# Kernel tuning notes

Hardware: AMD Instinct MI355X
Metric: run time of the kernel (lower is better)

## Reference

```python
import jax, jax.numpy as jnp
import numpy as np

B, S, D, H, DFF = 4, 2048, 1024, 16, 4096
DK = D // H
EPS = 1e-6


def setup_inputs() -> dict:
    key = jax.random.key(0)
    ks = jax.random.split(key, 20)
    p = lambda k, shape: jax.random.normal(k, shape, dtype=jnp.float32) * 0.02
    inp = {
        "x": jax.random.normal(ks[0], (B, S, D), dtype=jnp.float32),
        "src_mask": jax.random.randint(ks[1], (B, 1, 1, S), 0, 2, dtype=jnp.int32),
        "Wq": p(ks[2], (D, D)), "bq": jnp.zeros((D,), jnp.float32),
        "Wk": p(ks[3], (D, D)), "bk": jnp.zeros((D,), jnp.float32),
        "Wv": p(ks[4], (D, D)), "bv": jnp.zeros((D,), jnp.float32),
        "Wo": p(ks[5], (D, D)), "bo": jnp.zeros((D,), jnp.float32),
        "W1": p(ks[6], (D, DFF)), "b1": jnp.zeros((DFF,), jnp.float32),
        "W2": p(ks[7], (DFF, D)), "b2": jnp.zeros((D,), jnp.float32),
        "ln1_a": jnp.ones((D,), jnp.float32), "ln1_b": jnp.zeros((D,), jnp.float32),
        "ln2_a": jnp.ones((D,), jnp.float32), "ln2_b": jnp.zeros((D,), jnp.float32),
    }
    return inp


def _layer_norm(x, a, b):
    # Faithful to source: unbiased std (torch default) and divide by (std + eps)
    mean = jnp.mean(x, axis=-1, keepdims=True)
    std = jnp.std(x, axis=-1, ddof=1, keepdims=True)
    return a * (x - mean) / (std + EPS) + b


def reference(x, src_mask, Wq, bq, Wk, bk, Wv, bv, Wo, bo, W1, b1, W2, b2,
              ln1_a, ln1_b, ln2_a, ln2_b):
    # Multi-head self-attention (dropout = identity, eval mode)
    q = (x @ Wq + bq).reshape(B, S, H, DK)
    k = (x @ Wk + bk).reshape(B, S, H, DK)
    v = (x @ Wv + bv).reshape(B, S, H, DK)
    scores = jnp.einsum("bqhd,bkhd->bhqk", q, k) / jnp.sqrt(jnp.float32(DK))
    scores = jnp.where(src_mask == 0, jnp.float32(-1e9), scores)
    attn = jax.nn.softmax(scores, axis=-1)
    ctx = jnp.einsum("bhqk,bkhd->bqhd", attn, v).reshape(B, S, D)
    attn_out = ctx @ Wo + bo

    x = _layer_norm(x + attn_out, ln1_a, ln1_b)

    # FeedForward: linear -> relu -> (dropout=identity) -> linear
    ff = jax.nn.relu(x @ W1 + b1) @ W2 + b2
    x = _layer_norm(x + ff, ln2_a, ln2_b)
    return x
```

## Files before the change

kernel.cpp:

```cpp
#include <hip/hip_runtime.h>

#define Bn 4
#define Sn 2048
#define Dn 1024
#define Hn 16
#define DKn 64
#define DFFn 4096
#define Mn (Bn * Sn)
#define QKVS 3072

typedef __bf16 bf16;
typedef __attribute__((ext_vector_type(8))) __bf16 bf16x8;
typedef __attribute__((ext_vector_type(4))) __bf16 bf16x4;
typedef __attribute__((ext_vector_type(8))) unsigned short u16x8;
typedef __attribute__((ext_vector_type(4))) float f32x4;
typedef __attribute__((ext_vector_type(16))) float f32x16;

#define LOG2E_DIV8 0.18033688011112042f

__device__ __forceinline__ float exp2fast(float x) {
  return __builtin_amdgcn_exp2f(x);
}

__device__ __forceinline__ void glds16(const bf16* g, bf16* l) {
  __builtin_amdgcn_global_load_lds((const __attribute__((address_space(1))) void*)g,
                                   (__attribute__((address_space(3))) void*)l, 16, 0, 0);
}

__device__ __forceinline__ unsigned int pkbf16(float a, float b) {
  union { __bf16 h[2]; unsigned int u; } x;
  x.h[0] = (__bf16)a; x.h[1] = (__bf16)b;
  return x.u;
}

__device__ __host__ __forceinline__ int bperm(int nl) {
  int wn = nl >> 6, rem = nl & 63, nf = rem >> 4, l = rem & 15;
  return ((nf >> 1) << 7) + (wn << 5) + ((nf & 1) << 4) + l;
}

__global__ __launch_bounds__(256) void k_cvt_bf16(const float* __restrict__ in,
                                                  bf16* __restrict__ out) {
  size_t i = ((size_t)blockIdx.x * 256 + threadIdx.x) * 8;
  f32x4 a = *(const f32x4*)(in + i);
  f32x4 b = *(const f32x4*)(in + i + 4);
  bf16x8 o;
#pragma unroll
  for (int j = 0; j < 4; ++j) { o[j] = (bf16)a[j]; o[j + 4] = (bf16)b[j]; }
  *(bf16x8*)(out + i) = o;
}

__global__ __launch_bounds__(256) void k_prep(const float* __restrict__ Wq,
                                              const float* __restrict__ Wk,
                                              const float* __restrict__ Wv,
                                              const float* __restrict__ Wo,
                                              const float* __restrict__ W1,
                                              const float* __restrict__ W2,
                                              const float* __restrict__ bq,
                                              const float* __restrict__ bk,
                                              const float* __restrict__ bv,
                                              bf16* __restrict__ wqkvT,
                                              bf16* __restrict__ woT,
                                              bf16* __restrict__ w1T,
                                              bf16* __restrict__ w2T,
                                              float* __restrict__ bqkv) {
  __shared__ float tile[32][33];
  const int id = blockIdx.x, t = threadIdx.x;
  if (id >= 12288) {
    int j = (id - 12288) * 256 + t;
    float v = (j < 1024) ? bq[j] * LOG2E_DIV8
            : (j < 2048) ? bk[j - 1024] : bv[j - 2048];
    bqkv[j] = v;
    return;
  }
  const float* in;
  bf16* out;
  int K, N, bx, by, perm;
  float scale = 1.f;
  if (id < 4096) {
    int z = id >> 10, local = id & 1023;
    bx = local & 31; by = local >> 5;
    K = Dn; N = Dn;
    if (z == 0)      { in = Wq; out = wqkvT; scale = LOG2E_DIV8; perm = 1; }
    else if (z == 1) { in = Wk; out = wqkvT + (size_t)1024 * Dn; perm = 1; }
    else if (z == 2) { in = Wv; out = wqkvT + (size_t)2048 * Dn; perm = 1; }
    else             { in = Wo; out = woT; perm = 0; }
  } else if (id < 8192) {
    int local = id - 4096;
    bx = local & 127; by = local >> 7;
    K = Dn; N = DFFn; in = W1; out = w1T; perm = 1;
  } else {
    int local = id - 8192;
    bx = local & 31; by = local >> 5;
    K = DFFn; N = Dn; in = W2; out = w2T; perm = 0;
  }
  const int n0 = bx * 32, k0 = by * 32;
  const int tx = t & 31, ty = t >> 5;
#pragma unroll
  for (int j = ty; j < 32; j += 8)
    tile[j][tx] = in[(size_t)(k0 + j) * N + n0 + tx];
  __syncthreads();
#pragma unroll
  for (int j = ty; j < 32; j += 8) {
    int row = n0 + j;
    if (perm) row = (row & ~255) | bperm(row & 255);
    out[(size_t)row * K + k0 + tx] = (bf16)(tile[tx][j] * scale);
  }
}

__global__ __launch_bounds__(256) void k_vt(const bf16* __restrict__ v,
                                            bf16* __restrict__ vT, int vs) {
  __shared__ bf16 T[64][72];
  const int t = threadIdx.x;
  const int s0 = blockIdx.x * 64;
  const int bh = blockIdx.y, b = bh >> 4, h = bh & 15;
#pragma unroll
  for (int it = 0; it < 2; ++it) {
    int r = (t >> 3) + it * 32;
    int c = t & 7;
    u16x8 val = *(const u16x8*)(v + (size_t)(b * Sn + s0 + r) * vs + h * 64 + c * 8);
    *(u16x8*)&T[r][c * 8] = val;
  }
  __syncthreads();
#pragma unroll
  for (int it = 0; it < 2; ++it) {
    int d = (t >> 3) + it * 32;
    int cs = t & 7;
    bf16x8 o;
#pragma unroll
    for (int j = 0; j < 8; ++j) o[j] = T[cs * 8 + j][d];
    *(bf16x8*)(vT + ((size_t)bh * 64 + d) * Sn + s0 + cs * 8) = o;
  }
}

template <int DO_RELU>
__global__ __launch_bounds__(512, 2) void k_gemm8ph(const bf16* __restrict__ A,
                                                    const bf16* __restrict__ BT,
                                                    const float* __restrict__ bias,
                                                    bf16* __restrict__ C,
                                                    int Ndim, int Kdim) {
  __shared__ __align__(128) bf16 Asm[2][256 * 64];
  __shared__ __align__(128) bf16 Bsm[2][256 * 64];
  const int tid = threadIdx.x;
  const int wid = tid >> 6, lane = tid & 63;
  const int l15 = lane & 15, l4 = lane >> 4;
  const int wm = wid >> 2, wn = wid & 3;

  const int gx = gridDim.x;
  int lin = blockIdx.y * gx + blockIdx.x;
  const int nwg = gx * gridDim.y;
  lin = (lin & 7) * (nwg >> 3) + (lin >> 3);
  const int m0 = (lin / gx) * 256;
  const int n0 = (lin % gx) * 256;

  f32x4 acc[8][4];
#pragma unroll
  for (int mf = 0; mf < 8; ++mf)
#pragma unroll
    for (int nf = 0; nf < 4; ++nf) acc[mf][nf] = f32x4{0.f, 0.f, 0.f, 0.f};

  const int lr = lane >> 3, lc = lane & 7;
  const int NT = Kdim >> 6;
  const int ch0 = lc ^ lr;

#define STGA(buf, t, it)                                                          \
  glds16(A + (size_t)(m0 + (it) * 64 + wid * 8 + lr) * Kdim + (size_t)(t) * 64 +  \
             ch0 * 8,                                                             \
         &Asm[buf][((it) * 64 + wid * 8) * 64]);
#define STGB(buf, t, it)                                                          \
  glds16(BT + (size_t)(n0 + (it) * 64 + wid * 8 + lr) * Kdim + (size_t)(t) * 64 + \
              ch0 * 8,                                                            \
         &Bsm[buf][((it) * 64 + wid * 8) * 64]);

  STGA(0, 0, 0); STGA(0, 0, 2);
  STGB(0, 0, 0); STGB(0, 0, 1);
  STGA(0, 0, 1); STGA(0, 0, 3);
  STGB(0, 0, 2); STGB(0, 0, 3);

  bf16x8 af[4][2], bl[2][2], bh2[2][2];

  for (int j = 0; j < NT; ++j) {
    const int d = j & 1, nb = d ^ 1;
    const bool st = (j + 1 < NT);

    asm volatile("s_waitcnt vmcnt(4)" ::: "memory");
    __builtin_amdgcn_sched_barrier(0);
    __builtin_amdgcn_s_barrier();
#pragma unroll
    for (int mf = 0; mf < 4; ++mf)
#pragma unroll
      for (int kk = 0; kk < 2; ++kk) {
        int row = wm * 128 + mf * 16 + l15;
        int ch = (kk * 4 + l4) ^ (row & 7);
        af[mf][kk] = *(const bf16x8*)&Asm[d][row * 64 + ch * 8];
      }
#pragma unroll
    for (int nf = 0; nf < 2; ++nf)
#pragma unroll
      for (int kk = 0; kk < 2; ++kk) {
        int row = wn * 32 + nf * 16 + l15;
        int ch = (kk * 4 + l4) ^ (row & 7);
        bl[nf][kk] = *(const bf16x8*)&Bsm[d][row * 64 + ch * 8];
      }
    if (st) { STGA(nb, j + 1, 0); STGA(nb, j + 1, 2); }
    __builtin_amdgcn_s_setprio(1);
#pragma unroll
    for (int mf = 0; mf < 4; ++mf)
#pragma unroll
      for (int nf = 0; nf < 2; ++nf)
#pragma unroll
        for (int kk = 0; kk < 2; ++kk)
          acc[mf][nf] = __builtin_amdgcn_mfma_f32_16x16x32_bf16(af[mf][kk], bl[nf][kk],
                                                                acc[mf][nf], 0, 0, 0);
    __builtin_amdgcn_s_setprio(0);

    if (st) asm volatile("s_waitcnt vmcnt(4)" ::: "memory");
    else    asm volatile("s_waitcnt vmcnt(2)" ::: "memory");
    __builtin_amdgcn_sched_barrier(0);
    __builtin_amdgcn_s_barrier();
#pragma unroll
    for (int mf = 0; mf < 4; ++mf)
#pragma unroll
      for (int kk = 0; kk < 2; ++kk) {
        int row = wm * 128 + 64 + mf * 16 + l15;
        int ch = (kk * 4 + l4) ^ (row & 7);
        af[mf][kk] = *(const bf16x8*)&Asm[d][row * 64 + ch * 8];
      }
    if (st) { STGB(nb, j + 1, 0); STGB(nb, j + 1, 1); }
    __builtin_amdgcn_s_setprio(1);
#pragma unroll
    for (int mf = 0; mf < 4; ++mf)
#pragma unroll
      for (int nf = 0; nf < 2; ++nf)
#pragma unroll
        for (int kk = 0; kk < 2; ++kk)
          acc[4 + mf][nf] = __builtin_amdgcn_mfma_f32_16x16x32_bf16(af[mf][kk], bl[nf][kk],
                                                                    acc[4 + mf][nf], 0, 0, 0);
    __builtin_amdgcn_s_setprio(0);

    if (st) asm volatile("s_waitcnt vmcnt(4)" ::: "memory");
    else    asm volatile("s_waitcnt vmcnt(0)" ::: "memory");
    __builtin_amdgcn_sched_barrier(0);
    __builtin_amdgcn_s_barrier();
#pragma unroll
    for (int nf = 0; nf < 2; ++nf)
#pragma unroll
      for (int kk = 0; kk < 2; ++kk) {
        int row = 128 + wn * 32 + nf * 16 + l15;
        int ch = (kk * 4 + l4) ^ (row & 7);
        bh2[nf][kk] = *(const bf16x8*)&Bsm[d][row * 64 + ch * 8];
      }
    if (st) { STGA(nb, j + 1, 1); STGA(nb, j + 1, 3); }
    __builtin_amdgcn_s_setprio(1);
#pragma unroll
    for (int mf = 0; mf < 4; ++mf)
#pragma unroll
      for (int nf = 0; nf < 2; ++nf)
#pragma unroll
        for (int kk = 0; kk < 2; ++kk)
          acc[4 + mf][2 + nf] = __builtin_amdgcn_mfma_f32_16x16x32_bf16(
              af[mf][kk], bh2[nf][kk], acc[4 + mf][2 + nf], 0, 0, 0);
    __builtin_amdgcn_s_setprio(0);

#pragma unroll
    for (int mf = 0; mf < 4; ++mf)
#pragma unroll
      for (int kk = 0; kk < 2; ++kk) {
        int row = wm * 128 + mf * 16 + l15;
        int ch = (kk * 4 + l4) ^ (row & 7);
        af[mf][kk] = *(const bf16x8*)&Asm[d][row * 64 + ch * 8];
      }
    if (st) { STGB(nb, j + 1, 2); STGB(nb, j + 1, 3); }
    __builtin_amdgcn_s_setprio(1);
#pragma unroll
    for (int mf = 0; mf < 4; ++mf)
#pragma unroll
      for (int nf = 0; nf < 2; ++nf)
#pragma unroll
        for (int kk = 0; kk < 2; ++kk)
          acc[mf][2 + nf] = __builtin_amdgcn_mfma_f32_16x16x32_bf16(
              af[mf][kk], bh2[nf][kk], acc[mf][2 + nf], 0, 0, 0);
    __builtin_amdgcn_s_setprio(0);
  }
#undef STGA
#undef STGB

#pragma unroll
  for (int mf = 0; mf < 8; ++mf)
#pragma unroll
    for (int nf = 0; nf < 4; ++nf) {
      int c = n0 + wn * 64 + nf * 16 + l15;
      float bv = bias[c];
      int r0 = m0 + wm * 128 + mf * 16 + l4 * 4;
#pragma unroll
      for (int r = 0; r < 4; ++r) {
        float val = acc[mf][nf][r] + bv;
        if (DO_RELU) val = fmaxf(val, 0.f);
        C[(size_t)(r0 + r) * Ndim + c] = (bf16)val;
      }
    }
}

template <int NFRAG, int DO_RELU>
__global__ __launch_bounds__(512, 2) void k_gemm256(const bf16* __restrict__ A,
                                                    const bf16* __restrict__ BT,
                                                    const float* __restrict__ bias,
                                                    bf16* __restrict__ C,
                                                    int Ndim, int Kdim) {
  __shared__ __align__(128) bf16 Asm[2][256 * 64];
  __shared__ __align__(128) bf16 Bsm[2][NFRAG * 64 * 64];
  const int tid = threadIdx.x;
  const int wid = tid >> 6, lane = tid & 63;
  const int l15 = lane & 15, l4 = lane >> 4;
  const int wm = wid >> 2, wn = wid & 3;

  const int gx = gridDim.x;
  int lin = blockIdx.y * gx + blockIdx.x;
  const int nwg = gx * gridDim.y;
  lin = (lin & 7) * (nwg >> 3) + (lin >> 3);
  const int m0 = (lin / gx) * 256;
  const int n0 = (lin % gx) * (NFRAG * 64);

  f32x4 acc[8][NFRAG];
#pragma unroll
  for (int mf = 0; mf < 8; ++mf)
#pragma unroll
    for (int nf = 0; nf < NFRAG; ++nf) acc[mf][nf] = f32x4{0.f, 0.f, 0.f, 0.f};

  const int lr = lane >> 3, lc = lane & 7;
  const int NT = Kdim >> 6;

#define STAGE(buf, t)                                                              \
  {                                                                                \
    _Pragma("unroll") for (int it = 0; it < 4; ++it) {                             \
      int r = it * 64 + wid * 8 + lr;                                              \
      int ch = lc ^ (r & 7);                                                       \
      glds16(A + (size_t)(m0 + r) * Kdim + (size_t)(t) * 64 + ch * 8,              \
             &Asm[buf][(it * 64 + wid * 8) * 64]);                                 \
    }                                                                              \
    _Pragma("unroll") for (int it = 0; it < NFRAG; ++it) {                         \
      int r = it * 64 + wid * 8 + lr;                                              \
      int ch = lc ^ (r & 7);                                                       \
      glds16(BT + (size_t)(n0 + r) * Kdim + (size_t)(t) * 64 + ch * 8,             \
             &Bsm[buf][(it * 64 + wid * 8) * 64]);                                 \
    }                                                                              \
  }

  int p = 0;
  STAGE(0, 0);
  for (int t = 0; t < NT; ++t) {
    if (t + 1 < NT) {
      STAGE(p ^ 1, t + 1);
      if constexpr (NFRAG == 4) asm volatile("s_waitcnt vmcnt(8)" ::: "memory");
      else                      asm volatile("s_waitcnt vmcnt(6)" ::: "memory");
    } else {
      asm volatile("s_waitcnt vmcnt(0)" ::: "memory");
    }
    __builtin_amdgcn_sched_barrier(0);
    __builtin_amdgcn_s_barrier();

    bf16x8 bfrag[NFRAG][2];
#pragma unroll
    for (int nf = 0; nf < NFRAG; ++nf)
#pragma unroll
      for (int kk = 0; kk < 2; ++kk) {
        int r = wn * (NFRAG * 16) + nf * 16 + l15;
        int ch = (kk * 4 + l4) ^ (r & 7);
        bfrag[nf][kk] = *(const bf16x8*)&Bsm[p][r * 64 + ch * 8];
      }
#pragma unroll
    for (int half = 0; half < 2; ++half) {
      bf16x8 afr[4][2];
#pragma unroll
      for (int mf4 = 0; mf4 < 4; ++mf4)
#pragma unroll
        for (int kk = 0; kk < 2; ++kk) {
          int r = wm * 128 + half * 64 + mf4 * 16 + l15;
          int ch = (kk * 4 + l4) ^ (r & 7);
          afr[mf4][kk] = *(const bf16x8*)&Asm[p][r * 64 + ch * 8];
        }
      __builtin_amdgcn_s_setprio(1);
#pragma unroll
      for (int mf4 = 0; mf4 < 4; ++mf4)
#pragma unroll
        for (int nf = 0; nf < NFRAG; ++nf)
#pragma unroll
          for (int kk = 0; kk < 2; ++kk)
            acc[half * 4 + mf4][nf] = __builtin_amdgcn_mfma_f32_16x16x32_bf16(
                afr[mf4][kk], bfrag[nf][kk], acc[half * 4 + mf4][nf], 0, 0, 0);
      __builtin_amdgcn_s_setprio(0);
    }
    __builtin_amdgcn_s_barrier();
    p ^= 1;
  }
#undef STAGE

#pragma unroll
  for (int mf = 0; mf < 8; ++mf)
#pragma unroll
    for (int nf = 0; nf < NFRAG; ++nf) {
      int c = n0 + wn * (NFRAG * 16) + nf * 16 + l15;
      float bv = bias[c];
      int r0 = m0 + wm * 128 + mf * 16 + l4 * 4;
#pragma unroll
      for (int r = 0; r < 4; ++r) {
        float val = acc[mf][nf][r] + bv;
        if (DO_RELU) val = fmaxf(val, 0.f);
        C[(size_t)(r0 + r) * Ndim + c] = (bf16)val;
      }
    }
}

__global__ __launch_bounds__(512) void k_attn(const bf16* __restrict__ q,
                                              const bf16* __restrict__ k,
                                              const bf16* __restrict__ vT,
                                              const int* __restrict__ mask,
                                              bf16* __restrict__ ctx, int qs) {
  __shared__ __align__(128) bf16 Kt[2][64 * 64];
  __shared__ __align__(128) bf16 Vt[2][64 * 64];
  __shared__ float Mb[Sn];
  const int tid = threadIdx.x, wid = tid >> 6, lane = tid & 63;
  const int q31 = lane & 31, hi = lane >> 5;

  int lin = blockIdx.y * gridDim.x + blockIdx.x;
  lin = (lin & 7) * 64 + (lin >> 3);
  const int qblk = lin & 7, bh = lin >> 3;
  const int b = bh >> 4, h = bh & 15;
  const int q0 = qblk * 256 + wid * 32;

  for (int i = tid; i < Sn; i += 512)
    Mb[i] = mask[b * Sn + i] ? 0.f : -1.44269504e9f;

  bf16x8 qf[4];
#pragma unroll
  for (int t = 0; t < 4; ++t)
    qf[t] = *(const bf16x8*)(q + (size_t)(b * Sn + q0 + q31) * qs + h * 64 +
                             t * 16 + hi * 8);

  f32x16 o[2];
  o[0] = {}; o[1] = {};
  float mr = -INFINITY, lr = 0.f;

  const int lrow = lane >> 3;
  const int lch0 = lane & 7;
  const int sch = lch0 ^ (lrow ^ (wid & 3));

  for (int kb = 0; kb < Sn / 64; ++kb) {
    const int cur = kb & 1;
    if (kb == 0) {
      int row = wid * 8 + lrow;
      glds16(k + (size_t)(b * Sn + row) * qs + h * 64 + sch * 8, &Kt[0][wid * 512]);
      glds16(vT + ((size_t)bh * 64 + row) * Sn + sch * 8, &Vt[0][wid * 512]);
      __syncthreads();
    }
    if (kb + 1 < Sn / 64) {
      int row = wid * 8 + lrow;
      glds16(k + (size_t)(b * Sn + (kb + 1) * 64 + row) * qs + h * 64 + sch * 8,
             &Kt[cur ^ 1][wid * 512]);
      glds16(vT + ((size_t)bh * 64 + row) * Sn + (kb + 1) * 64 + sch * 8,
             &Vt[cur ^ 1][wid * 512]);
    }

    f32x16 sc[2];
#pragma unroll
    for (int kf = 0; kf < 2; ++kf)
#pragma unroll
      for (int rg = 0; rg < 4; ++rg) {
        f32x4 mb4 = *(const f32x4*)&Mb[kb * 64 + kf * 32 + rg * 8 + 4 * hi];
#pragma unroll
        for (int j = 0; j < 4; ++j) sc[kf][rg * 4 + j] = mb4[j];
      }
#pragma unroll
    for (int t = 0; t < 4; ++t) {
#pragma unroll
      for (int kf = 0; kf < 2; ++kf) {
        int row = kf * 32 + q31;
        int ch = (t * 2 + hi) ^ ((row & 7) ^ ((row >> 3) & 3));
        bf16x8 kfr = *(const bf16x8*)&Kt[cur][row * 64 + ch * 8];
        sc[kf] = __builtin_amdgcn_mfma_f32_32x32x16_bf16(kfr, qf[t], sc[kf], 0, 0, 0);
      }
    }

    float rmax = fmaxf(sc[0][0], sc[0][1]);
#pragma unroll
    for (int i = 2; i < 16; i += 2)
      rmax = fmaxf(fmaxf(rmax, sc[0][i]), sc[0][i + 1]);
#pragma unroll
    for (int i = 0; i < 16; i += 2)
      rmax = fmaxf(fmaxf(rmax, sc[1][i]), sc[1][i + 1]);
    rmax = fmaxf(rmax, __shfl_xor(rmax, 32));

    if (!__all(rmax <= mr + 8.f)) {
      float mnew = fmaxf(mr, rmax);
      float psc = exp2fast(mr - mnew);
      mr = mnew;
      lr *= psc;
#pragma unroll
      for (int af = 0; af < 2; ++af)
#pragma unroll
        for (int i = 0; i < 16; ++i) o[af][i] *= psc;
    }

    float psum = 0.f;
#pragma unroll
    for (int kf = 0; kf < 2; ++kf)
#pragma unroll
      for (int i = 0; i < 16; ++i) {
        float p = exp2fast(sc[kf][i] - mr);
        sc[kf][i] = p;
        psum += p;
      }
    psum += __shfl_xor(psum, 32);
    lr += psum;

#pragma unroll
    for (int ks = 0; ks < 4; ++ks) {
      const int kf = ks >> 1, R = (ks & 1) * 8;
      unsigned int a0 = pkbf16(sc[kf][R + 0], sc[kf][R + 1]);
      unsigned int a1 = pkbf16(sc[kf][R + 2], sc[kf][R + 3]);
      unsigned int b0 = pkbf16(sc[kf][R + 4], sc[kf][R + 5]);
      unsigned int b1 = pkbf16(sc[kf][R + 6], sc[kf][R + 7]);
      unsigned int sxa0 = __shfl_xor(a0, 32), sxa1 = __shfl_xor(a1, 32);
      unsigned int sxb0 = __shfl_xor(b0, 32), sxb1 = __shfl_xor(b1, 32);
      union { unsigned int w[4]; bf16x8 v; } pfu;
      pfu.w[0] = hi ? sxb0 : a0;
      pfu.w[1] = hi ? sxb1 : a1;
      pfu.w[2] = hi ? b0 : sxa0;
      pfu.w[3] = hi ? b1 : sxa1;
#pragma unroll
      for (int af = 0; af < 2; ++af) {
        int row = af * 32 + q31;
        int ch = (ks * 2 + hi) ^ ((row & 7) ^ ((row >> 3) & 3));
        bf16x8 vfr = *(const bf16x8*)&Vt[cur][row * 64 + ch * 8];
        o[af] = __builtin_amdgcn_mfma_f32_32x32x16_bf16(vfr, pfu.v, o[af], 0, 0, 0);
      }
    }
    __syncthreads();
  }

  float inv = 1.f / lr;
  const size_t cbase = (size_t)(b * Sn + q0 + q31) * Dn + h * 64;
#pragma unroll
  for (int af = 0; af < 2; ++af)
#pragma unroll
    for (int rg = 0; rg < 4; ++rg) {
      bf16x4 ov;
#pragma unroll
      for (int j = 0; j < 4; ++j) ov[j] = (bf16)(o[af][rg * 4 + j] * inv);
      *(bf16x4*)(ctx + cbase + af * 32 + rg * 8 + 4 * hi) = ov;
    }
}

template <int XF32, int OUTF32>
__global__ __launch_bounds__(256) void k_ln(const void* __restrict__ xp,
                                            const bf16* __restrict__ res,
                                            const float* __restrict__ gamma,
                                            const float* __restrict__ beta,
                                            void* __restrict__ yout) {
  const int row = blockIdx.x, t = threadIdx.x;
  const size_t base = (size_t)row * Dn + t * 4;
  f32x4 a;
  if constexpr (XF32) {
    a = *(const f32x4*)((const float*)xp + base);
  } else {
    bf16x4 x4 = *(const bf16x4*)((const bf16*)xp + base);
#pragma unroll
    for (int j = 0; j < 4; ++j) a[j] = (float)x4[j];
  }
  bf16x4 rb = *(const bf16x4*)(res + base);
  f32x4 vv;
#pragma unroll
  for (int j = 0; j < 4; ++j) vv[j] = a[j] + (float)rb[j];

  float s = vv[0] + vv[1] + vv[2] + vv[3];
#pragma unroll
  for (int off = 32; off; off >>= 1) s += __shfl_xor(s, off);
  __shared__ float red1[4], red2[4];
  if ((t & 63) == 0) red1[t >> 6] = s;
  __syncthreads();
  float mean = (red1[0] + red1[1] + red1[2] + red1[3]) * (1.f / 1024.f);

  float d[4], s2 = 0.f;
#pragma unroll
  for (int j = 0; j < 4; ++j) { d[j] = vv[j] - mean; s2 += d[j] * d[j]; }
#pragma unroll
  for (int off = 32; off; off >>= 1) s2 += __shfl_xor(s2, off);
  if ((t & 63) == 0) red2[t >> 6] = s2;
  __syncthreads();
  float var = (red2[0] + red2[1] + red2[2] + red2[3]) * (1.f / 1023.f);
  float inv = 1.f / (sqrtf(var) + 1e-6f);

  f32x4 g = *(const f32x4*)(gamma + t * 4);
  f32x4 bt = *(const f32x4*)(beta + t * 4);
#pragma unroll
  for (int j = 0; j < 4; ++j) d[j] = g[j] * d[j] * inv + bt[j];
  if constexpr (OUTF32) {
    f32x4 outv = {d[0], d[1], d[2], d[3]};
    *(f32x4*)((float*)yout + base) = outv;
  } else {
    bf16x4 outb;
#pragma unroll
    for (int j = 0; j < 4; ++j) outb[j] = (bf16)d[j];
    *(bf16x4*)((bf16*)yout + base) = outb;
  }
}

extern "C" void kernel_launch(void* const* d_in, const int* in_sizes, int n_in,
                              void* d_out, int out_size, void* d_ws, size_t ws_size,
                              hipStream_t stream) {
  const float* x   = (const float*)d_in[0];
  const int*   msk = (const int*)d_in[1];
  const float* Wq  = (const float*)d_in[2];
  const float* bq  = (const float*)d_in[3];
  const float* Wk  = (const float*)d_in[4];
  const float* bk  = (const float*)d_in[5];
  const float* Wv  = (const float*)d_in[6];
  const float* bv  = (const float*)d_in[7];
  const float* Wo  = (const float*)d_in[8];
  const float* bo  = (const float*)d_in[9];
  const float* W1  = (const float*)d_in[10];
  const float* b1  = (const float*)d_in[11];
  const float* W2  = (const float*)d_in[12];
  const float* b2  = (const float*)d_in[13];
  const float* g1  = (const float*)d_in[14];
  const float* be1 = (const float*)d_in[15];
  const float* g2  = (const float*)d_in[16];
  const float* be2 = (const float*)d_in[17];
  float* out = (float*)d_out;

  char* w = (char*)d_ws;
  size_t off = 0;
  auto alloc = [&](size_t bytes) { void* p = w + off; off += (bytes + 255) & ~(size_t)255; return p; };
  bf16* xb    = (bf16*)alloc((size_t)Mn * Dn * 2);
  bf16* wqkvT = (bf16*)alloc((size_t)QKVS * Dn * 2);
  bf16* woT   = (bf16*)alloc((size_t)Dn * Dn * 2);
  bf16* w1T   = (bf16*)alloc((size_t)Dn * DFFn * 2);
  bf16* w2T   = (bf16*)alloc((size_t)DFFn * Dn * 2);
  float* bqkv = (float*)alloc((size_t)QKVS * 4);
  bf16* qkv   = (bf16*)alloc((size_t)Mn * QKVS * 2);
  bf16* ctx   = (bf16*)alloc((size_t)Mn * Dn * 2);
  bf16* attnb = (bf16*)alloc((size_t)Mn * Dn * 2);
  bf16* yb    = (bf16*)alloc((size_t)Mn * Dn * 2);
  (void)ws_size; (void)in_sizes; (void)n_in; (void)out_size;
  bf16* vT = xb;
  bf16* hh = qkv;
  bf16* ff = xb;

  k_cvt_bf16<<<(Mn * Dn) / 2048, 256, 0, stream>>>(x, xb);
  k_prep<<<12300, 256, 0, stream>>>(Wq, Wk, Wv, Wo, W1, W2, bq, bk, bv,
                                    wqkvT, woT, w1T, w2T, bqkv);

  k_gemm8ph<0><<<dim3(QKVS / 256, Mn / 256), 512, 0, stream>>>(xb, wqkvT, bqkv, qkv, QKVS, Dn);

  k_vt<<<dim3(Sn / 64, Bn * Hn), 256, 0, stream>>>(qkv + 2048, vT, QKVS);
  k_attn<<<dim3(Sn / 256, Bn * Hn), 512, 0, stream>>>(qkv, qkv + 1024, vT, msk, ctx, QKVS);

  k_gemm256<2, 0><<<dim3(Dn / 128, Mn / 256), 512, 0, stream>>>(ctx, woT, bo, attnb, Dn, Dn);

  k_ln<1, 0><<<Mn, 256, 0, stream>>>(x, attnb, g1, be1, yb);

  k_gemm8ph<1><<<dim3(DFFn / 256, Mn / 256), 512, 0, stream>>>(yb, w1T, b1, hh, DFFn, Dn);

  k_gemm256<2, 0><<<dim3(Dn / 128, Mn / 256), 512, 0, stream>>>(hh, w2T, b2, ff, Dn, DFFn);

  k_ln<0, 1><<<Mn, 256, 0, stream>>>(yb, ff, g2, be2, out);
}
```

Measured before the change: 399.0 us.

## Split attention KV range in two halves and merge with combine kernel

Applies a flash-decoding-style split: each attention block now processes half of the key/value sequence, doubling the grid from 512 to 1024 blocks, and writes unnormalized partial outputs plus running max/sum. A new combine kernel rescales and merges the two partials into the normalized context. This aims to improve occupancy and load balance across the GPU's compute units, at the cost of extra partial-output traffic (bf16 partials, extra rounding) and one more kernel launch.

```diff
diff --git a/kernel.cpp b/kernel.cpp
--- a/kernel.cpp
+++ b/kernel.cpp
@@ -414,7 +414,8 @@
                                               const bf16* __restrict__ k,
                                               const bf16* __restrict__ vT,
                                               const int* __restrict__ mask,
-                                              bf16* __restrict__ ctx, int qs) {
+                                              bf16* __restrict__ opart,
+                                              float2* __restrict__ ml, int qs) {
   __shared__ __align__(128) bf16 Kt[2][64 * 64];
   __shared__ __align__(128) bf16 Vt[2][64 * 64];
   __shared__ float Mb[Sn];
@@ -422,10 +423,12 @@
   const int q31 = lane & 31, hi = lane >> 5;
 
   int lin = blockIdx.y * gridDim.x + blockIdx.x;
-  lin = (lin & 7) * 64 + (lin >> 3);
-  const int qblk = lin & 7, bh = lin >> 3;
+  lin = (lin & 7) * 128 + (lin >> 3);
+  const int xq = lin & 15, bh = lin >> 4;
+  const int half = xq & 1, qblk = xq >> 1;
   const int b = bh >> 4, h = bh & 15;
   const int q0 = qblk * 256 + wid * 32;
+  const int kv0 = half * 16;
 
   for (int i = tid; i < Sn; i += 512)
     Mb[i] = mask[b * Sn + i] ? 0.f : -1.44269504e9f;
@@ -444,15 +447,17 @@
   const int lch0 = lane & 7;
   const int sch = lch0 ^ (lrow ^ (wid & 3));
 
-  for (int kb = 0; kb < Sn / 64; ++kb) {
-    const int cur = kb & 1;
-    if (kb == 0) {
+  for (int t16 = 0; t16 < 16; ++t16) {
+    const int kb = kv0 + t16;
+    const int cur = t16 & 1;
+    if (t16 == 0) {
       int row = wid * 8 + lrow;
-      glds16(k + (size_t)(b * Sn + row) * qs + h * 64 + sch * 8, &Kt[0][wid * 512]);
-      glds16(vT + ((size_t)bh * 64 + row) * Sn + sch * 8, &Vt[0][wid * 512]);
+      glds16(k + (size_t)(b * Sn + kb * 64 + row) * qs + h * 64 + sch * 8,
+             &Kt[0][wid * 512]);
+      glds16(vT + ((size_t)bh * 64 + row) * Sn + kb * 64 + sch * 8, &Vt[0][wid * 512]);
       __syncthreads();
     }
-    if (kb + 1 < Sn / 64) {
+    if (t16 + 1 < 16) {
       int row = wid * 8 + lrow;
       glds16(k + (size_t)(b * Sn + (kb + 1) * 64 + row) * qs + h * 64 + sch * 8,
              &Kt[cur ^ 1][wid * 512]);
@@ -537,17 +542,40 @@
     __syncthreads();
   }
 
-  float inv = 1.f / lr;
-  const size_t cbase = (size_t)(b * Sn + q0 + q31) * Dn + h * 64;
+  const size_t row = (size_t)(b * Sn + q0 + q31);
+  const size_t obase = ((size_t)half * Mn + row) * Dn + h * 64;
 #pragma unroll
   for (int af = 0; af < 2; ++af)
 #pragma unroll
     for (int rg = 0; rg < 4; ++rg) {
       bf16x4 ov;
 #pragma unroll
-      for (int j = 0; j < 4; ++j) ov[j] = (bf16)(o[af][rg * 4 + j] * inv);
-      *(bf16x4*)(ctx + cbase + af * 32 + rg * 8 + 4 * hi) = ov;
-    }
+      for (int j = 0; j < 4; ++j) ov[j] = (bf16)o[af][rg * 4 + j];
+      *(bf16x4*)(opart + obase + af * 32 + rg * 8 + 4 * hi) = ov;
+    }
+  if (lane < 32) ml[((size_t)half * Mn + row) * Hn + h] = float2{mr, lr};
+}
+
+__global__ __launch_bounds__(256) void k_combine(const bf16* __restrict__ opart,
+                                                 const float2* __restrict__ ml,
+                                                 bf16* __restrict__ ctx) {
+  int idx = blockIdx.x * 256 + threadIdx.x;
+  int row = idx >> 8;
+  int c4 = idx & 255;
+  int h = c4 >> 4;
+  float2 m0 = ml[(size_t)row * Hn + h];
+  float2 m1 = ml[((size_t)Mn + row) * Hn + h];
+  float m = fmaxf(m0.x, m1.x);
+  float a0 = exp2fast(m0.x - m), a1 = exp2fast(m1.x - m);
+  float inv = 1.f / (a0 * m0.y + a1 * m1.y);
+  size_t off = (size_t)row * Dn + c4 * 4;
+  bf16x4 o0 = *(const bf16x4*)(opart + off);
+  bf16x4 o1 = *(const bf16x4*)(opart + (size_t)Mn * Dn + off);
+  bf16x4 o;
+#pragma unroll
+  for (int j = 0; j < 4; ++j)
+    o[j] = (bf16)((a0 * (float)o0[j] + a1 * (float)o1[j]) * inv);
+  *(bf16x4*)(ctx + off) = o;
 }
 
 template <int XF32, int OUTF32>
@@ -640,6 +668,8 @@
   bf16* ctx   = (bf16*)alloc((size_t)Mn * Dn * 2);
   bf16* attnb = (bf16*)alloc((size_t)Mn * Dn * 2);
   bf16* yb    = (bf16*)alloc((size_t)Mn * Dn * 2);
+  bf16* opart = (bf16*)alloc((size_t)2 * Mn * Dn * 2);
+  float2* mlb = (float2*)alloc((size_t)2 * Mn * Hn * 8);
   (void)ws_size; (void)in_sizes; (void)n_in; (void)out_size;
   bf16* vT = xb;
   bf16* hh = qkv;
@@ -652,7 +682,8 @@
   k_gemm8ph<0><<<dim3(QKVS / 256, Mn / 256), 512, 0, stream>>>(xb, wqkvT, bqkv, qkv, QKVS, Dn);
 
   k_vt<<<dim3(Sn / 64, Bn * Hn), 256, 0, stream>>>(qkv + 2048, vT, QKVS);
-  k_attn<<<dim3(Sn / 256, Bn * Hn), 512, 0, stream>>>(qkv, qkv + 1024, vT, msk, ctx, QKVS);
+  k_attn<<<dim3(16, Bn * Hn), 512, 0, stream>>>(qkv, qkv + 1024, vT, msk, opart, mlb, QKVS);
+  k_combine<<<(Mn * Dn / 4) / 256, 256, 0, stream>>>(opart, mlb, ctx);
 
   k_gemm256<2, 0><<<dim3(Dn / 128, Mn / 256), 512, 0, stream>>>(ctx, woT, bo, attnb, Dn, Dn);
 
```

Result: slower. 417.3 us (+4.6%).
